# Kernel tuning notes

Hardware: AMD Instinct MI355X
Metric: run time of the kernel (lower is better)

Reference implementation:

```python
import jax, jax.numpy as jnp
import numpy as np


def _conv(x, w):
    # NCHW 'same' conv, stride 1 (kernel 7 -> pad 3 each side)
    return jax.lax.conv_general_dilated(
        x, w, window_strides=(1, 1), padding='SAME',
        dimension_numbers=('NCHW', 'OIHW', 'NCHW'))


def _run_dir(x, w_ih, w_hh, b, reverse):
    # x: (B, T, C, H, W); returns (B, T, hid, H, W)
    B, T, C, H, W = x.shape
    hid = w_hh.shape[1]
    # Precompute input-to-gate convs for all timesteps at once (fold T into batch)
    xg = _conv(x.reshape(B * T, C, H, W), w_ih) + b[None, :, None, None]
    xg = xg.reshape(B, T, 4 * hid, H, W).transpose(1, 0, 2, 3, 4)  # (T,B,4hid,H,W)
    h0 = jnp.zeros((B, hid, H, W), x.dtype)
    c0 = jnp.zeros_like(h0)

    def step(carry, g_x):
        h, c = carry
        g = g_x + _conv(h, w_hh)
        i, f, gg, o = jnp.split(g, 4, axis=1)  # PyTorch LSTM gate order
        c = jax.nn.sigmoid(f) * c + jax.nn.sigmoid(i) * jnp.tanh(gg)
        h = jax.nn.sigmoid(o) * jnp.tanh(c)
        return (h, c), h

    _, hs = jax.lax.scan(step, (h0, c0), xg, reverse=reverse)
    return hs.transpose(1, 0, 2, 3, 4)  # (B,T,hid,H,W)


def setup_inputs() -> dict:
    key = jax.random.key(0)
    ks = jax.random.split(key, 6)
    B, T, C, H, W = 8, 16, 3, 32, 32
    hid, K = 64, 7
    s_ih = 1.0 / np.sqrt(C * K * K)
    s_hh = 1.0 / np.sqrt(hid * K * K)
    return {
        'x': jax.random.normal(ks[0], (B, T, C, H, W), jnp.float32),
        'w_ih_f': jax.random.normal(ks[1], (4 * hid, C, K, K), jnp.float32) * s_ih,
        'w_hh_f': jax.random.normal(ks[2], (4 * hid, hid, K, K), jnp.float32) * s_hh,
        'b_f': jnp.zeros((4 * hid,), jnp.float32),
        'w_ih_b': jax.random.normal(ks[3], (4 * hid, C, K, K), jnp.float32) * s_ih,
        'w_hh_b': jax.random.normal(ks[4], (4 * hid, hid, K, K), jnp.float32) * s_hh,
        'b_b': jnp.zeros((4 * hid,), jnp.float32),
    }


def reference(x, w_ih_f, w_hh_f, b_f, w_ih_b, w_hh_b, b_b):
    out_f = _run_dir(x, w_ih_f, w_hh_f, b_f, reverse=False)
    out_b = _run_dir(x, w_ih_b, w_hh_b, b_b, reverse=True)
    # bidirectional concat along channel dim -> (B, T, 2*hid, H, W)
    return jnp.concatenate([out_f, out_b], axis=2)
```

## Files before the change

kernel.cpp:

```cpp
#include <hip/hip_runtime.h>
#include <hip/hip_bf16.h>


#define HP0_B  0
#define HP1_B  3112960
#define C_B    6225920
#define WALL_B 10420224
#define BIAS_B 13860864
#define FLAG_B 13862912

#define AOFF   26240
#define LDS_BYTES 118016

using short8 = __attribute__((ext_vector_type(8))) short;
using f32x4  = __attribute__((ext_vector_type(4))) float;

__device__ __forceinline__ float sigm(float x) { return 1.0f / (1.0f + __expf(-x)); }
__device__ __forceinline__ float tanh_f(float x) {
    x = fminf(fmaxf(x, -30.0f), 30.0f);
    float e = __expf(2.0f * x);
    return (e - 1.0f) / (e + 1.0f);
}

__global__ void detect_dtype(const unsigned int* __restrict__ xw, int* __restrict__ flag) {
    int lane = threadIdx.x;
    int cnt = 0;
    for (int i = 0; i < 4; ++i) {
        unsigned int w = xw[lane * 4 + i];
        unsigned int e = (w >> 7) & 0xFFu;
        cnt += (e >= 0xC0u) ? 1 : 0;
    }
#pragma unroll
    for (int off = 32; off > 0; off >>= 1) cnt += __shfl_down(cnt, off, 64);
    if (lane == 0) *flag = (cnt > 16) ? 1 : 0;
}

__global__ void prep_weights(const void* __restrict__ whhf, const void* __restrict__ whhb,
                             const void* __restrict__ wihf, const void* __restrict__ wihb,
                             const void* __restrict__ bf, const void* __restrict__ bb,
                             short* __restrict__ wall, float* __restrict__ bias_r,
                             const int* __restrict__ flag) {
    int n = blockIdx.x * blockDim.x + threadIdx.x;
    const int fp32 = *flag;
    if (n < 1720320) {
        int icl = n & 31;
        int oc = (n >> 5) & 255;
        int ks = (n >> 13) % 105;
        int d = n / 860160;
        const void* hh = d ? whhb : whhf;
        const void* ih = d ? wihb : wihf;
        float v = 0.0f;
        if (ks < 98) {
            int ky = ks / 14, rr = ks % 14, kc = rr / 7, kx = rr % 7;
            int si = ((oc * 64 + kc * 32 + icl) * 7 + ky) * 7 + kx;
            v = fp32 ? ((const float*)hh)[si] : __bfloat162float(((const __hip_bfloat16*)hh)[si]);
        } else {
            int kx = ks - 98, ky = icl >> 2, ic = icl & 3;
            if (ic < 3 && ky < 7) {
                int si = ((oc * 3 + ic) * 7 + ky) * 7 + kx;
                v = fp32 ? ((const float*)ih)[si] : __bfloat162float(((const __hip_bfloat16*)ih)[si]);
            }
        }
        __hip_bfloat16 hv = __float2bfloat16(v);
        wall[n] = *(short*)&hv;
        return;
    }
    n -= 1720320;
    if (n < 512) {
        const void* src = (n >= 256) ? bb : bf;
        int j = n & 255;
        bias_r[n] = fp32 ? ((const float*)src)[j] : __bfloat162float(((const __hip_bfloat16*)src)[j]);
    }
}

__global__ void zero_state(float* __restrict__ ws_f) {
    int n = blockIdx.x * blockDim.x + threadIdx.x;
    if (n < 2605056) ws_f[n] = 0.0f;
}

#define WAITV(n) asm volatile("s_waitcnt vmcnt(" #n ")" ::: "memory")

__global__ __launch_bounds__(256, 1)
void lstm_step(const void* __restrict__ xin,
               const short* __restrict__ wall,
               const float* __restrict__ bias_r,
               const unsigned short* __restrict__ hp_r,
               unsigned short* __restrict__ hp_w,
               float* __restrict__ c,
               void* __restrict__ out,
               const int* __restrict__ flag, int s) {
    extern __shared__ short lds[];
    const int bid = blockIdx.x;
    const int dir = bid & 1;
    const int b = (bid >> 1) & 7;
    const int ygrp = bid >> 4;
    const int t = dir ? (15 - s) : s;
    const int y0 = ygrp * 2;
    const int tid = threadIdx.x;
    const int wv = tid >> 6;
    const int l = tid & 63;
    const int q = l >> 4;
    const int li = l & 15;
    const int fp32 = *flag;
    const int db = dir * 8 + b;

    const short* wdir = wall + (size_t)dir * 860160;

    const int glane = (wv * 16 + li) * 32 + q * 8;
    const int lwave = AOFF + wv * 2048;

    auto stageA = [&](int ks) {
        const short* gp = wdir + (size_t)ks * 8192 + glane;
        short* lp = &lds[lwave + ((ks & 3) << 13)];
#pragma unroll
        for (int g = 0; g < 4; ++g) {
            __builtin_amdgcn_global_load_lds(
                (const __attribute__((address_space(1))) int*)(gp + g * 2048),
                (__attribute__((address_space(3))) int*)(lp + g * 512),
                16, 0, 0);
        }
    };

    stageA(0); stageA(1); stageA(2);

    {
        const uint4* src = (const uint4*)(hp_r + (size_t)(db * 38 + y0) * 40 * 64);
        for (int i = tid; i < 2560; i += 256) {
            int ic8 = i & 7, col = (i >> 3) % 40, row = i / 320;
            uint4 v = src[i];
            *(uint4*)&lds[(row * 40 + col) * 72 + ic8 * 8] = v;
        }
    }
    for (int i = tid; i < 3200; i += 256) {
        int k = i % 40, cc = (i / 40) % 40, r = i / 1600;
        float v = 0.0f;
        if (k < 28) {
            int ky = k >> 2, ic = k & 3;
            int yin = y0 + r + ky - 3, cin = cc - 3;
            if (ic < 3 && yin >= 0 && yin < 32 && cin >= 0 && cin < 32) {
                size_t gi = (size_t)((b * 16 + t) * 3 + ic) * 1024 + yin * 32 + cin;
                v = fp32 ? ((const float*)xin)[gi]
                         : __bfloat162float(((const __hip_bfloat16*)xin)[gi]);
            }
        }
        __hip_bfloat16 hb = __float2bfloat16(v);
        lds[23040 + i] = *(short*)&hb;
    }
    __syncthreads();

    f32x4 acc[4][4];
    {
        const float* bp = bias_r + dir * 256 + wv * 16 + q * 4;
#pragma unroll
        for (int g = 0; g < 4; ++g) {
            f32x4 bv = *(const f32x4*)(bp + g * 64);
#pragma unroll
            for (int nt = 0; nt < 4; ++nt) acc[g][nt] = bv;
        }
    }

    int bh[4], bx[4];
#pragma unroll
    for (int nt = 0; nt < 4; ++nt) {
        int rt = nt >> 1, ct = nt & 1;
        bh[nt] = (rt * 40 + ct * 16 + li) * 72 + q * 8;
        bx[nt] = 23040 + (rt * 40 + ct * 16 + li) * 40 + q * 8;
    }

    auto loadA = [&](short8* A, int ks) {
        const short* p = &lds[lwave + ((ks & 3) << 13) + l * 8];
#pragma unroll
        for (int g = 0; g < 4; ++g) A[g] = *(const short8*)(p + g * 512);
    };
    auto loadB = [&](short8* B, int ks) {
        if (ks < 98) {
            int ky = ks / 14, rr = ks % 14;
            int uoff = ky * 2880 + (rr % 7) * 72 + (rr / 7) * 32;
#pragma unroll
            for (int nt = 0; nt < 4; ++nt) B[nt] = *(const short8*)&lds[bh[nt] + uoff];
        } else {
            int uoff = (ks - 98) * 40;
#pragma unroll
            for (int nt = 0; nt < 4; ++nt) B[nt] = *(const short8*)&lds[bx[nt] + uoff];
        }
    };
    auto mfma16 = [&](short8* A, short8* B) {
        __builtin_amdgcn_s_setprio(1);
#pragma unroll
        for (int g = 0; g < 4; ++g)
#pragma unroll
            for (int nt = 0; nt < 4; ++nt)
                acc[g][nt] = __builtin_amdgcn_mfma_f32_16x16x32_bf16(A[g], B[nt], acc[g][nt], 0, 0, 0);
        __builtin_amdgcn_s_setprio(0);
    };

    short8 Aa[4], Ba[4], Ab[4], Bb[4];
    loadA(Aa, 0); loadB(Ba, 0);
#pragma unroll 1
    for (int ks = 0; ks < 102; ks += 2) {
        stageA(ks + 3);
        WAITV(8);
        loadA(Ab, ks + 1); loadB(Bb, ks + 1);
        mfma16(Aa, Ba);
        stageA(ks + 4);
        WAITV(8);
        loadA(Aa, ks + 2); loadB(Ba, ks + 2);
        mfma16(Ab, Bb);
    }
    WAITV(4);
    loadA(Ab, 103); loadB(Bb, 103);
    mfma16(Aa, Ba);
    WAITV(0);
    loadA(Aa, 104); loadB(Ba, 104);
    mfma16(Ab, Bb);
    mfma16(Aa, Ba);

    const int hid0 = wv * 16 + q * 4;
#pragma unroll
    for (int nt = 0; nt < 4; ++nt) {
        int y = y0 + (nt >> 1);
        int px = (nt & 1) * 16 + li;
        float* cp = c + (size_t)(db * 1024 + y * 32 + px) * 64 + hid0;
        f32x4 cold = *(const f32x4*)cp;
        f32x4 hv;
#pragma unroll
        for (int r = 0; r < 4; ++r) {
            float iv = sigm(acc[0][nt][r]);
            float fv = sigm(acc[1][nt][r]);
            float gv = tanh_f(acc[2][nt][r]);
            float ov = sigm(acc[3][nt][r]);
            float cn = fv * cold[r] + iv * gv;
            cold[r] = cn;
            hv[r] = ov * tanh_f(cn);
        }
        *(f32x4*)cp = cold;

        ushort4 hu;
        {
            __hip_bfloat16 t0 = __float2bfloat16(hv[0]); hu.x = *(unsigned short*)&t0;
            __hip_bfloat16 t1 = __float2bfloat16(hv[1]); hu.y = *(unsigned short*)&t1;
            __hip_bfloat16 t2 = __float2bfloat16(hv[2]); hu.z = *(unsigned short*)&t2;
            __hip_bfloat16 t3 = __float2bfloat16(hv[3]); hu.w = *(unsigned short*)&t3;
        }
        *(ushort4*)(hp_w + (size_t)((db * 38 + y + 3) * 40 + px + 3) * 64 + hid0) = hu;

        size_t ob = (size_t)((b * 16 + t) * 128 + dir * 64 + hid0) * 1024 + y * 32 + px;
        if (fp32) {
            float* op = (float*)out;
#pragma unroll
            for (int r = 0; r < 4; ++r) op[ob + (size_t)r * 1024] = hv[r];
        } else {
            __hip_bfloat16* op = (__hip_bfloat16*)out;
#pragma unroll
            for (int r = 0; r < 4; ++r) op[ob + (size_t)r * 1024] = __float2bfloat16(hv[r]);
        }
    }
}

__global__ __launch_bounds__(512, 2)
void lstm_step_fb(const void* __restrict__ xin,
                  const short* __restrict__ wall,
                  const float* __restrict__ bias_r,
                  const unsigned short* __restrict__ hp_r,
                  unsigned short* __restrict__ hp_w,
                  float* __restrict__ c,
                  void* __restrict__ out,
                  const int* __restrict__ flag, int s) {
    const int bid = blockIdx.x;
    const int dir = bid & 1;
    const int b = (bid >> 1) & 7;
    const int ygrp = bid >> 4;
    const int t = dir ? (15 - s) : s;
    const int y0 = ygrp * 2;
    const int tid = threadIdx.x;
    const int wv = tid >> 6;
    const int kg = wv >> 2;
    const int wm = wv & 3;
    const int l = tid & 63;
    const int q = l >> 4;
    const int li = l & 15;
    const int fp32 = *flag;
    const int db = dir * 8 + b;

    __shared__ __align__(16) short lds[26240];

    {
        const uint4* src = (const uint4*)(hp_r + (size_t)(db * 38 + y0) * 40 * 64);
        for (int i = tid; i < 2560; i += 512) {
            int ic8 = i & 7, col = (i >> 3) % 40, row = i / 320;
            uint4 v = src[i];
            *(uint4*)&lds[(row * 40 + col) * 72 + ic8 * 8] = v;
        }
    }
    for (int i = tid; i < 3200; i += 512) {
        int k = i % 40, cc = (i / 40) % 40, r = i / 1600;
        float v = 0.0f;
        if (k < 28) {
            int ky = k >> 2, ic = k & 3;
            int yin = y0 + r + ky - 3, cin = cc - 3;
            if (ic < 3 && yin >= 0 && yin < 32 && cin >= 0 && cin < 32) {
                size_t gi = (size_t)((b * 16 + t) * 3 + ic) * 1024 + yin * 32 + cin;
                v = fp32 ? ((const float*)xin)[gi]
                         : __bfloat162float(((const __hip_bfloat16*)xin)[gi]);
            }
        }
        __hip_bfloat16 hb = __float2bfloat16(v);
        lds[23040 + i] = *(short*)&hb;
    }
    __syncthreads();

    f32x4 acc[4][4];
    if (kg == 0) {
        const float* bp = bias_r + dir * 256 + wm * 16 + q * 4;
#pragma unroll
        for (int g = 0; g < 4; ++g) {
            f32x4 bv = *(const f32x4*)(bp + g * 64);
#pragma unroll
            for (int nt = 0; nt < 4; ++nt) acc[g][nt] = bv;
        }
    } else {
        f32x4 z = {0.0f, 0.0f, 0.0f, 0.0f};
#pragma unroll
        for (int g = 0; g < 4; ++g)
#pragma unroll
            for (int nt = 0; nt < 4; ++nt) acc[g][nt] = z;
    }

    const short* wbase = wall + (size_t)dir * 860160 + ((wm * 16 + li) * 32 + q * 8);
    int bh[4], bx[4];
#pragma unroll
    for (int nt = 0; nt < 4; ++nt) {
        int rt = nt >> 1, ct = nt & 1;
        bh[nt] = (rt * 40 + ct * 16 + li) * 72 + q * 8;
        bx[nt] = 23040 + (rt * 40 + ct * 16 + li) * 40 + q * 8;
    }

    auto loadA = [&](short8* A, int ks) {
        const short* p = wbase + (size_t)ks * 8192;
#pragma unroll
        for (int g = 0; g < 4; ++g) A[g] = *(const short8*)(p + g * 2048);
    };
    auto loadB = [&](short8* B, int ks) {
        if (ks < 98) {
            int ky = ks / 14, rr = ks % 14;
            int uoff = ky * 2880 + (rr % 7) * 72 + (rr / 7) * 32;
#pragma unroll
            for (int nt = 0; nt < 4; ++nt) B[nt] = *(const short8*)&lds[bh[nt] + uoff];
        } else {
            int uoff = (ks - 98) * 40;
#pragma unroll
            for (int nt = 0; nt < 4; ++nt) B[nt] = *(const short8*)&lds[bx[nt] + uoff];
        }
    };
    auto mfma16 = [&](short8* A, short8* B) {
        __builtin_amdgcn_s_setprio(1);
#pragma unroll
        for (int g = 0; g < 4; ++g)
#pragma unroll
            for (int nt = 0; nt < 4; ++nt)
                acc[g][nt] = __builtin_amdgcn_mfma_f32_16x16x32_bf16(A[g], B[nt], acc[g][nt], 0, 0, 0);
        __builtin_amdgcn_s_setprio(0);
    };

    const int ks_begin = kg ? 52 : 0;
    const int ks_end   = kg ? 105 : 52;
    short8 A0[4], A1[4], B0[4], B1[4];
    loadA(A0, ks_begin); loadB(B0, ks_begin);
    int ks = ks_begin;
#pragma unroll 1
    for (; ks + 1 < ks_end; ks += 2) {
        loadA(A1, ks + 1); loadB(B1, ks + 1);
        mfma16(A0, B0);
        int kn = (ks + 2 < ks_end) ? ks + 2 : ks;
        loadA(A0, kn); loadB(B0, kn);
        mfma16(A1, B1);
    }
    if (ks < ks_end) mfma16(A0, B0);

    __syncthreads();
    {
        float* exch = (float*)lds;
        float* xp = exch + wm * 2048 + q * 64 + li * 4;
        if (kg == 1) {
#pragma unroll
            for (int g = 0; g < 2; ++g)
#pragma unroll
                for (int nt = 0; nt < 4; ++nt)
                    *(f32x4*)(xp + (g * 4 + nt) * 256) = acc[g][nt];
        }
        __syncthreads();
        if (kg == 0) {
#pragma unroll
            for (int g = 0; g < 2; ++g)
#pragma unroll
                for (int nt = 0; nt < 4; ++nt)
                    acc[g][nt] += *(const f32x4*)(xp + (g * 4 + nt) * 256);
        }
        __syncthreads();
        if (kg == 1) {
#pragma unroll
            for (int g = 0; g < 2; ++g)
#pragma unroll
                for (int nt = 0; nt < 4; ++nt)
                    *(f32x4*)(xp + (g * 4 + nt) * 256) = acc[2 + g][nt];
        }
        __syncthreads();
        if (kg == 0) {
#pragma unroll
            for (int g = 0; g < 2; ++g)
#pragma unroll
                for (int nt = 0; nt < 4; ++nt)
                    acc[2 + g][nt] += *(const f32x4*)(xp + (g * 4 + nt) * 256);
        }
    }
    if (kg == 1) return;

    const int hid0 = wm * 16 + q * 4;
#pragma unroll
    for (int nt = 0; nt < 4; ++nt) {
        int y = y0 + (nt >> 1);
        int px = (nt & 1) * 16 + li;
        float* cp = c + (size_t)(db * 1024 + y * 32 + px) * 64 + hid0;
        f32x4 cold = *(const f32x4*)cp;
        f32x4 hv;
#pragma unroll
        for (int r = 0; r < 4; ++r) {
            float iv = sigm(acc[0][nt][r]);
            float fv = sigm(acc[1][nt][r]);
            float gv = tanh_f(acc[2][nt][r]);
            float ov = sigm(acc[3][nt][r]);
            float cn = fv * cold[r] + iv * gv;
            cold[r] = cn;
            hv[r] = ov * tanh_f(cn);
        }
        *(f32x4*)cp = cold;

        ushort4 hu;
        {
            __hip_bfloat16 t0 = __float2bfloat16(hv[0]); hu.x = *(unsigned short*)&t0;
            __hip_bfloat16 t1 = __float2bfloat16(hv[1]); hu.y = *(unsigned short*)&t1;
            __hip_bfloat16 t2 = __float2bfloat16(hv[2]); hu.z = *(unsigned short*)&t2;
            __hip_bfloat16 t3 = __float2bfloat16(hv[3]); hu.w = *(unsigned short*)&t3;
        }
        *(ushort4*)(hp_w + (size_t)((db * 38 + y + 3) * 40 + px + 3) * 64 + hid0) = hu;

        size_t ob = (size_t)((b * 16 + t) * 128 + dir * 64 + hid0) * 1024 + y * 32 + px;
        if (fp32) {
            float* op = (float*)out;
#pragma unroll
            for (int r = 0; r < 4; ++r) op[ob + (size_t)r * 1024] = hv[r];
        } else {
            __hip_bfloat16* op = (__hip_bfloat16*)out;
#pragma unroll
            for (int r = 0; r < 4; ++r) op[ob + (size_t)r * 1024] = __float2bfloat16(hv[r]);
        }
    }
}

extern "C" void kernel_launch(void* const* d_in, const int* in_sizes, int n_in,
                              void* d_out, int out_size, void* d_ws, size_t ws_size,
                              hipStream_t stream) {
    char* wsb = (char*)d_ws;
    unsigned short* hp0 = (unsigned short*)(wsb + HP0_B);
    unsigned short* hp1 = (unsigned short*)(wsb + HP1_B);
    float* c = (float*)(wsb + C_B);
    short* wall = (short*)(wsb + WALL_B);
    float* bias_r = (float*)(wsb + BIAS_B);
    int* flag = (int*)(wsb + FLAG_B);

    static int big_lds_ok = -1;
    if (big_lds_ok < 0) {
        hipError_t e = hipFuncSetAttribute((const void*)lstm_step,
                                           hipFuncAttributeMaxDynamicSharedMemorySize,
                                           LDS_BYTES);
        big_lds_ok = (e == hipSuccess) ? 1 : 0;
    }

    detect_dtype<<<1, 64, 0, stream>>>((const unsigned int*)d_in[0], flag);
    prep_weights<<<6722, 256, 0, stream>>>(d_in[2], d_in[5], d_in[1], d_in[4],
                                           d_in[3], d_in[6], wall, bias_r, flag);
    zero_state<<<10176, 256, 0, stream>>>((float*)d_ws);

    if (big_lds_ok) {
        for (int s = 0; s < 16; ++s) {
            unsigned short* hr = (s & 1) ? hp1 : hp0;
            unsigned short* hw = (s & 1) ? hp0 : hp1;
            lstm_step<<<dim3(256), 256, LDS_BYTES, stream>>>(d_in[0], wall, bias_r,
                                                             hr, hw, c, d_out, flag, s);
        }
    } else {
        for (int s = 0; s < 16; ++s) {
            unsigned short* hr = (s & 1) ? hp1 : hp0;
            unsigned short* hw = (s & 1) ? hp0 : hp1;
            lstm_step_fb<<<dim3(256), 512, 0, stream>>>(d_in[0], wall, bias_r,
                                                        hr, hw, c, d_out, flag, s);
        }
    }
}
```

Baseline: 725.9 us.

## Split hidden channels across blocks and load weights directly from global memory

Each block now owns a quarter of the hidden channels (mq) for eight output rows instead of all channels for two rows. Each wave takes two rows and reads its weight fragments straight from global/L2, dropping the async global-to-LDS weight staging pipeline and its explicit waitcnts. This cuts the weight slice each block needs to a quarter and lowers LDS use. In exchange, the larger h/x halo staged per block is loaded redundantly by the four mq blocks, and weight loads are no longer latency-hidden through LDS.

```diff
diff --git a/kernel.cpp b/kernel.cpp
--- a/kernel.cpp
+++ b/kernel.cpp
@@ -9,8 +9,8 @@
 #define BIAS_B 13860864
 #define FLAG_B 13862912
 
-#define AOFF   26240
-#define LDS_BYTES 118016
+#define XBOFF  40320
+#define LDS_BYTES 106240
 
 using short8 = __attribute__((ext_vector_type(8))) short;
 using f32x4  = __attribute__((ext_vector_type(4))) float;
@@ -78,60 +78,41 @@
     if (n < 2605056) ws_f[n] = 0.0f;
 }
 
-#define WAITV(n) asm volatile("s_waitcnt vmcnt(" #n ")" ::: "memory")
-
 __global__ __launch_bounds__(256, 1)
-void lstm_step(const void* __restrict__ xin,
-               const short* __restrict__ wall,
-               const float* __restrict__ bias_r,
-               const unsigned short* __restrict__ hp_r,
-               unsigned short* __restrict__ hp_w,
-               float* __restrict__ c,
-               void* __restrict__ out,
-               const int* __restrict__ flag, int s) {
+void lstm_step_mq(const void* __restrict__ xin,
+                  const short* __restrict__ wall,
+                  const float* __restrict__ bias_r,
+                  const unsigned short* __restrict__ hp_r,
+                  unsigned short* __restrict__ hp_w,
+                  float* __restrict__ c,
+                  void* __restrict__ out,
+                  const int* __restrict__ flag, int s) {
     extern __shared__ short lds[];
     const int bid = blockIdx.x;
     const int dir = bid & 1;
-    const int b = (bid >> 1) & 7;
-    const int ygrp = bid >> 4;
+    const int mq = (bid >> 1) & 3;
+    const int b = (bid >> 3) & 7;
+    const int yg = bid >> 6;
     const int t = dir ? (15 - s) : s;
-    const int y0 = ygrp * 2;
+    const int y0 = yg * 8;
     const int tid = threadIdx.x;
     const int wv = tid >> 6;
+    const int ry = 2 * wv;
     const int l = tid & 63;
     const int q = l >> 4;
     const int li = l & 15;
     const int fp32 = *flag;
     const int db = dir * 8 + b;
 
-    const short* wdir = wall + (size_t)dir * 860160;
-
-    const int glane = (wv * 16 + li) * 32 + q * 8;
-    const int lwave = AOFF + wv * 2048;
-
-    auto stageA = [&](int ks) {
-        const short* gp = wdir + (size_t)ks * 8192 + glane;
-        short* lp = &lds[lwave + ((ks & 3) << 13)];
-#pragma unroll
-        for (int g = 0; g < 4; ++g) {
-            __builtin_amdgcn_global_load_lds(
-                (const __attribute__((address_space(1))) int*)(gp + g * 2048),
-                (__attribute__((address_space(3))) int*)(lp + g * 512),
-                16, 0, 0);
-        }
-    };
-
-    stageA(0); stageA(1); stageA(2);
-
     {
         const uint4* src = (const uint4*)(hp_r + (size_t)(db * 38 + y0) * 40 * 64);
-        for (int i = tid; i < 2560; i += 256) {
+        for (int i = tid; i < 4480; i += 256) {
             int ic8 = i & 7, col = (i >> 3) % 40, row = i / 320;
             uint4 v = src[i];
             *(uint4*)&lds[(row * 40 + col) * 72 + ic8 * 8] = v;
         }
     }
-    for (int i = tid; i < 3200; i += 256) {
+    for (int i = tid; i < 12800; i += 256) {
         int k = i % 40, cc = (i / 40) % 40, r = i / 1600;
         float v = 0.0f;
         if (k < 28) {
@@ -144,13 +125,13 @@
             }
         }
         __hip_bfloat16 hb = __float2bfloat16(v);
-        lds[23040 + i] = *(short*)&hb;
+        lds[XBOFF + i] = *(short*)&hb;
     }
     __syncthreads();
 
     f32x4 acc[4][4];
     {
-        const float* bp = bias_r + dir * 256 + wv * 16 + q * 4;
+        const float* bp = bias_r + dir * 256 + mq * 16 + q * 4;
 #pragma unroll
         for (int g = 0; g < 4; ++g) {
             f32x4 bv = *(const f32x4*)(bp + g * 64);
@@ -159,18 +140,19 @@
         }
     }
 
+    const short* wbase = wall + (size_t)dir * 860160 + ((mq * 16 + li) * 32 + q * 8);
     int bh[4], bx[4];
 #pragma unroll
     for (int nt = 0; nt < 4; ++nt) {
         int rt = nt >> 1, ct = nt & 1;
-        bh[nt] = (rt * 40 + ct * 16 + li) * 72 + q * 8;
-        bx[nt] = 23040 + (rt * 40 + ct * 16 + li) * 40 + q * 8;
+        bh[nt] = ((ry + rt) * 40 + ct * 16 + li) * 72 + q * 8;
+        bx[nt] = XBOFF + ((ry + rt) * 40 + ct * 16 + li) * 40 + q * 8;
     }
 
     auto loadA = [&](short8* A, int ks) {
-        const short* p = &lds[lwave + ((ks & 3) << 13) + l * 8];
-#pragma unroll
-        for (int g = 0; g < 4; ++g) A[g] = *(const short8*)(p + g * 512);
+        const short* p = wbase + (size_t)ks * 8192;
+#pragma unroll
+        for (int g = 0; g < 4; ++g) A[g] = *(const short8*)(p + g * 2048);
     };
     auto loadB = [&](short8* B, int ks) {
         if (ks < 98) {
@@ -194,31 +176,22 @@
         __builtin_amdgcn_s_setprio(0);
     };
 
-    short8 Aa[4], Ba[4], Ab[4], Bb[4];
-    loadA(Aa, 0); loadB(Ba, 0);
+    short8 A0[4], A1[4], B0[4], B1[4];
+    loadA(A0, 0); loadB(B0, 0);
 #pragma unroll 1
-    for (int ks = 0; ks < 102; ks += 2) {
-        stageA(ks + 3);
-        WAITV(8);
-        loadA(Ab, ks + 1); loadB(Bb, ks + 1);
-        mfma16(Aa, Ba);
-        stageA(ks + 4);
-        WAITV(8);
-        loadA(Aa, ks + 2); loadB(Ba, ks + 2);
-        mfma16(Ab, Bb);
-    }
-    WAITV(4);
-    loadA(Ab, 103); loadB(Bb, 103);
-    mfma16(Aa, Ba);
-    WAITV(0);
-    loadA(Aa, 104); loadB(Ba, 104);
-    mfma16(Ab, Bb);
-    mfma16(Aa, Ba);
-
-    const int hid0 = wv * 16 + q * 4;
+    for (int ks = 0; ks < 104; ks += 2) {
+        loadA(A1, ks + 1); loadB(B1, ks + 1);
+        mfma16(A0, B0);
+        int kn = (ks + 2 < 105) ? ks + 2 : ks;
+        loadA(A0, kn); loadB(B0, kn);
+        mfma16(A1, B1);
+    }
+    mfma16(A0, B0);
+
+    const int hid0 = mq * 16 + q * 4;
 #pragma unroll
     for (int nt = 0; nt < 4; ++nt) {
-        int y = y0 + (nt >> 1);
+        int y = y0 + ry + (nt >> 1);
         int px = (nt & 1) * 16 + li;
         float* cp = c + (size_t)(db * 1024 + y * 32 + px) * 64 + hid0;
         f32x4 cold = *(const f32x4*)cp;
@@ -470,7 +443,7 @@
 
     static int big_lds_ok = -1;
     if (big_lds_ok < 0) {
-        hipError_t e = hipFuncSetAttribute((const void*)lstm_step,
+        hipError_t e = hipFuncSetAttribute((const void*)lstm_step_mq,
                                            hipFuncAttributeMaxDynamicSharedMemorySize,
                                            LDS_BYTES);
         big_lds_ok = (e == hipSuccess) ? 1 : 0;
@@ -485,8 +458,8 @@
         for (int s = 0; s < 16; ++s) {
             unsigned short* hr = (s & 1) ? hp1 : hp0;
             unsigned short* hw = (s & 1) ? hp0 : hp1;
-            lstm_step<<<dim3(256), 256, LDS_BYTES, stream>>>(d_in[0], wall, bias_r,
-                                                             hr, hw, c, d_out, flag, s);
+            lstm_step_mq<<<dim3(256), 256, LDS_BYTES, stream>>>(d_in[0], wall, bias_r,
+                                                                hr, hw, c, d_out, flag, s);
         }
     } else {
         for (int s = 0; s < 16; ++s) {
```

New measurement: 855.5 us. 17.9% more time.
